# Kernel optimization log

Measured on AMD Instinct MI355X. Metric: run time of the kernel, lower is better.

The kernel has to match this reference:

```python
import jax, jax.numpy as jnp
import numpy as np

N, F_IN, H, C, E = 100000, 128, 128, 40, 600000


def setup_inputs() -> dict:
    key = jax.random.key(0)
    ks = jax.random.split(key, 20)
    s = 0.05
    inp = {
        "x": jax.random.normal(ks[0], (N, F_IN), jnp.float32),
        "edge_index": jax.random.randint(ks[1], (2, E), 0, N, jnp.int64),
        "importance": jnp.ones((F_IN,), jnp.float32),
        "W1": jax.random.normal(ks[2], (H, F_IN), jnp.float32) * s,
        "bl1": jax.random.normal(ks[3], (H,), jnp.float32) * s,
        "bc1": jnp.zeros((H,), jnp.float32),
        "W2": jax.random.normal(ks[4], (H, H), jnp.float32) * s,
        "bl2": jax.random.normal(ks[5], (H,), jnp.float32) * s,
        "bc2": jnp.zeros((H,), jnp.float32),
        "W3": jax.random.normal(ks[6], (H, H), jnp.float32) * s,
        "bl3": jax.random.normal(ks[7], (H,), jnp.float32) * s,
        "bc3": jnp.zeros((H,), jnp.float32),
        "Wlin1": jax.random.normal(ks[8], (H, H), jnp.float32) * s,
        "blin1": jax.random.normal(ks[9], (H,), jnp.float32) * s,
        "Wlin2": jax.random.normal(ks[10], (C, H), jnp.float32) * s,
        "blin2": jax.random.normal(ks[11], (C,), jnp.float32) * s,
    }
    return inp


def balanced_conv(x, W, bl, bc, row, col):
    # lin, then symmetric-normalized message, mean-aggregated over targets
    n = x.shape[0]
    h = x @ W.T + bl                                   # [N, H]
    loops = jnp.arange(n)
    r = jnp.concatenate([row, loops])                  # sources (x_j index)
    c = jnp.concatenate([col, loops])                  # targets
    deg = jnp.zeros((n,), x.dtype).at[c].add(1.0)      # degree(col) incl. self-loops
    dinv = deg ** -0.5
    norm = dinv[r] * dinv[c]                           # [E+N]
    msg = norm[:, None] * h[r]                         # gather + scale
    agg = jnp.zeros((n, h.shape[1]), x.dtype).at[c].add(msg)  # scatter-add
    return agg / deg[:, None] + bc                     # mean aggr + bias


def reference(x, edge_index, importance, W1, bl1, bc1, W2, bl2, bc2,
              W3, bl3, bc3, Wlin1, blin1, Wlin2, blin2):
    row, col = edge_index[0], edge_index[1]
    h = x * importance
    h = jax.nn.relu(balanced_conv(h, W1, bl1, bc1, row, col))
    h = jax.nn.relu(balanced_conv(h, W2, bl2, bc2, row, col))
    h = jax.nn.relu(balanced_conv(h, W3, bl3, bc3, row, col))
    h = jax.nn.relu(h @ Wlin1.T + blin1)
    h = h @ Wlin2.T + blin2
    return jax.nn.log_softmax(h, axis=-1)
```

## Files before the change

kernel.cpp:

```cpp
#include <hip/hip_runtime.h>
#include <hip/hip_bf16.h>

#define F 128
#define C_CLS 40
#define NWSPLIT 35
#define ELLCAP 32

typedef __attribute__((ext_vector_type(8))) short short8;
typedef __attribute__((ext_vector_type(4))) float float4v;
typedef unsigned short ushort;

__device__ inline float bf2f(ushort u) {
  unsigned int x = ((unsigned int)u) << 16;
  return __builtin_bit_cast(float, x);
}
__device__ inline ushort f2bf(float f) {
  __hip_bfloat16 h = __float2bfloat16(f);
  return __builtin_bit_cast(ushort, h);
}
__device__ inline void split_bf16(float f, ushort& hi, ushort& lo) {
  hi = f2bf(f);
  lo = f2bf(f - bf2f(hi));
}
__device__ inline int swz(int lane) { return lane ^ ((lane >> 4) & 3); }

__global__ __launch_bounds__(256) void setup_kernel(
    const float* __restrict__ W1, const float* __restrict__ imp,
    const float* __restrict__ W2, const float* __restrict__ W3,
    const float* __restrict__ Wl1, const float* __restrict__ Wh2,
    ushort* __restrict__ WhP,
    ushort* __restrict__ W2hH, ushort* __restrict__ W2lH,
    const int* __restrict__ row, const int* __restrict__ col,
    int* __restrict__ cnt, int* __restrict__ ell,
    int ne, int n) {
  int b = blockIdx.x;
  if (b < NWSPLIT) {
    int ci = b * 256 + threadIdx.x;
    if (ci < 8192) {
      const float* src[4] = {W1, W2, W3, Wl1};
      int p = ci >> 11, c = ci & 2047;
      int kc = c >> 10, ct = (c >> 7) & 7, ks = (c >> 6) & 1, ln = c & 63;
      int dl = swz(ln);
      int colw = ct * 16 + (dl & 15);
      int k = kc * 64 + ks * 32 + (dl >> 4) * 8;
      float4 f0 = *(const float4*)&src[p][(size_t)colw * F + k];
      float4 f1 = *(const float4*)&src[p][(size_t)colw * F + k + 4];
      float v[8] = {f0.x, f0.y, f0.z, f0.w, f1.x, f1.y, f1.z, f1.w};
      if (p == 0) {
        float4 i0 = *(const float4*)&imp[k];
        float4 i1 = *(const float4*)&imp[k + 4];
        v[0] *= i0.x; v[1] *= i0.y; v[2] *= i0.z; v[3] *= i0.w;
        v[4] *= i1.x; v[5] *= i1.y; v[6] *= i1.z; v[7] *= i1.w;
      }
      ushort hi[8];
#pragma unroll
      for (int j = 0; j < 8; ++j) hi[j] = f2bf(v[j]);
      *(short8*)&WhP[(size_t)ci * 8] = *(short8*)hi;
    } else if (ci < 8192 + 768) {
      int c = ci - 8192;
      int ct = c >> 8, ks = (c >> 6) & 3, ln = c & 63;
      int colw = ct * 16 + (ln & 15);
      int k = ks * 32 + (ln >> 4) * 8;
      float v[8];
      if (colw < C_CLS) {
        float4 f0 = *(const float4*)&Wh2[(size_t)colw * F + k];
        float4 f1 = *(const float4*)&Wh2[(size_t)colw * F + k + 4];
        v[0] = f0.x; v[1] = f0.y; v[2] = f0.z; v[3] = f0.w;
        v[4] = f1.x; v[5] = f1.y; v[6] = f1.z; v[7] = f1.w;
      } else {
#pragma unroll
        for (int j = 0; j < 8; ++j) v[j] = 0.f;
      }
      ushort hi[8], lo[8];
#pragma unroll
      for (int j = 0; j < 8; ++j) split_bf16(v[j], hi[j], lo[j]);
      *(short8*)&W2hH[(size_t)c * 8] = *(short8*)hi;
      *(short8*)&W2lH[(size_t)c * 8] = *(short8*)lo;
    }
  } else {
    int e = (b - NWSPLIT) * 256 + threadIdx.x;
    if (e < ne) {
      int r = row[e], c = col[e];
      int p = atomicAdd(&cnt[c], 1);
      if (p < ELLCAP) ell[(size_t)c * ELLCAP + p] = r;
    }
  }
}

template <bool F32IN>
__global__ __launch_bounds__(256, 2) void gemm_any(const void* __restrict__ INv,
    const ushort* __restrict__ Wh,
    const float* __restrict__ bias, ushort* __restrict__ OUT, int nrows, int relu,
    int nbMain, const int* __restrict__ cntv, float* __restrict__ dinvv,
    float* __restrict__ invdegv, int n) {
  __shared__ ushort sWh[16384];
  if (blockIdx.x >= nbMain) {
    int i = (blockIdx.x - nbMain) * 256 + threadIdx.x;
    if (i < n) {
      float d = (float)(cntv[i] + 1);
      dinvv[i] = rsqrtf(d);
      invdegv[i] = 1.0f / d;
    }
    return;
  }
  const int t = threadIdx.x;
  const int rbase = blockIdx.x * 256;
  const int w = t >> 6, lane = t & 63;
  const int quad = lane >> 4, cl = lane & 15;

#pragma unroll
  for (int pp = 0; pp < 8; ++pp) {
    int ci = t + pp * 256;
    *(short8*)&sWh[ci * 8] = *(const short8*)&Wh[(size_t)ci * 8];
  }
  __syncthreads();

  float4v acc[4][8];
#pragma unroll
  for (int nt = 0; nt < 4; ++nt)
#pragma unroll
    for (int mt = 0; mt < 8; ++mt) acc[nt][mt] = (float4v){0.f, 0.f, 0.f, 0.f};

  const int sl = swz(lane);
  const int nrow0 = rbase + w * 64 + cl;
#pragma unroll
  for (int ks = 0; ks < 4; ++ks) {
    short8 b[4];
#pragma unroll
    for (int nt = 0; nt < 4; ++nt) {
      int gr = nrow0 + nt * 16;
      if (gr < nrows) {
        if (F32IN) {
          const float* INf = (const float*)INv;
          float4 f0 = *(const float4*)&INf[(size_t)gr * F + ks * 32 + quad * 8];
          float4 f1 = *(const float4*)&INf[(size_t)gr * F + ks * 32 + quad * 8 + 4];
          ushort h[8] = {f2bf(f0.x), f2bf(f0.y), f2bf(f0.z), f2bf(f0.w),
                         f2bf(f1.x), f2bf(f1.y), f2bf(f1.z), f2bf(f1.w)};
          b[nt] = *(short8*)h;
        } else {
          const ushort* IN = (const ushort*)INv;
          b[nt] = *(const short8*)&IN[(size_t)gr * F + ks * 32 + quad * 8];
        }
      } else {
        b[nt] = (short8){0, 0, 0, 0, 0, 0, 0, 0};
      }
    }
    const int base = ((ks >> 1) * 1024 + (ks & 1) * 64 + sl) * 8;
#pragma unroll
    for (int mt = 0; mt < 8; ++mt) {
      short8 a_h = *(short8*)&sWh[base + mt * 128 * 8];
#pragma unroll
      for (int nt = 0; nt < 4; ++nt)
        acc[nt][mt] = __builtin_amdgcn_mfma_f32_16x16x32_bf16(a_h, b[nt], acc[nt][mt], 0, 0, 0);
    }
  }
#pragma unroll
  for (int mt = 0; mt < 8; ++mt) {
    float4 bv = *(const float4*)&bias[mt * 16 + quad * 4];
#pragma unroll
    for (int nt = 0; nt < 4; ++nt) {
      int gr = nrow0 + nt * 16;
      if (gr < nrows) {
        float v0 = acc[nt][mt][0] + bv.x;
        float v1 = acc[nt][mt][1] + bv.y;
        float v2 = acc[nt][mt][2] + bv.z;
        float v3 = acc[nt][mt][3] + bv.w;
        if (relu) {
          v0 = fmaxf(v0, 0.f); v1 = fmaxf(v1, 0.f);
          v2 = fmaxf(v2, 0.f); v3 = fmaxf(v3, 0.f);
        }
        ushort o[4] = {f2bf(v0), f2bf(v1), f2bf(v2), f2bf(v3)};
        *(ushort4*)&OUT[(size_t)gr * F + mt * 16 + quad * 4] = *(ushort4*)o;
      }
    }
  }
}

__global__ __launch_bounds__(256) void gather_kernel(const int* __restrict__ cntv,
    const int* __restrict__ ell, const ushort* __restrict__ B,
    const float* __restrict__ dinv, const float* __restrict__ invdeg,
    const float* __restrict__ bc, ushort* __restrict__ A, int n) {
  int node = blockIdx.x * 16 + (threadIdx.x >> 4);
  if (node >= n) return;
  int j = (threadIdx.x & 15) * 8;
  int cnt = cntv[node];
  int lim = cnt < ELLCAP ? cnt : ELLCAP;
  float dc = dinv[node];
  const int4* ep = (const int4*)&ell[(size_t)node * ELLCAP];
  float a0[8] = {0, 0, 0, 0, 0, 0, 0, 0};
  float a1[8] = {0, 0, 0, 0, 0, 0, 0, 0};
  float a2[8] = {0, 0, 0, 0, 0, 0, 0, 0};
  float a3[8] = {0, 0, 0, 0, 0, 0, 0, 0};
  for (int base = 0; base < lim; base += 4) {
    int4 rr = ep[base >> 2];
    bool p1 = base + 1 < lim, p2 = base + 2 < lim, p3 = base + 3 < lim;
    int r1 = p1 ? rr.y : rr.x;
    int r2 = p2 ? rr.z : rr.x;
    int r3 = p3 ? rr.w : rr.x;
    float g0 = dinv[rr.x];
    float g1 = p1 ? dinv[r1] : 0.f;
    float g2 = p2 ? dinv[r2] : 0.f;
    float g3 = p3 ? dinv[r3] : 0.f;
    short8 v0 = *(const short8*)&B[(size_t)rr.x * F + j];
    short8 v1 = *(const short8*)&B[(size_t)r1 * F + j];
    short8 v2 = *(const short8*)&B[(size_t)r2 * F + j];
    short8 v3 = *(const short8*)&B[(size_t)r3 * F + j];
#pragma unroll
    for (int q = 0; q < 8; ++q) {
      a0[q] += g0 * bf2f((ushort)v0[q]);
      a1[q] += g1 * bf2f((ushort)v1[q]);
      a2[q] += g2 * bf2f((ushort)v2[q]);
      a3[q] += g3 * bf2f((ushort)v3[q]);
    }
  }
  float id = invdeg[node];
  short8 sv = *(const short8*)&B[(size_t)node * F + j];
  float4 b0 = *(const float4*)&bc[j];
  float4 b1 = *(const float4*)&bc[j + 4];
  float bcv[8] = {b0.x, b0.y, b0.z, b0.w, b1.x, b1.y, b1.z, b1.w};
  ushort o[8];
#pragma unroll
  for (int q = 0; q < 8; ++q) {
    float s = dc * ((a0[q] + a1[q]) + (a2[q] + a3[q]));
    o[q] = f2bf(fmaxf((s + bf2f((ushort)sv[q]) * id) * id + bcv[q], 0.f));
  }
  *(short8*)&A[(size_t)node * F + j] = *(short8*)o;
}

__global__ __launch_bounds__(256, 2) void head_fused(const ushort* __restrict__ X,
    const ushort* __restrict__ Wl1h, const float* __restrict__ bl,
    const ushort* __restrict__ W2h, const ushort* __restrict__ W2l,
    const float* __restrict__ b2, float* __restrict__ out, int nrows) {
  __shared__ ushort sWh[16384];
  __shared__ ushort sW2h[6144], sW2l[6144];
  __shared__ ushort sH[8192];
  __shared__ float b2s[48];
  const int t = threadIdx.x;
#pragma unroll
  for (int pp = 0; pp < 8; ++pp) {
    int ci = t + pp * 256;
    *(short8*)&sWh[ci * 8] = *(const short8*)&Wl1h[(size_t)ci * 8];
  }
#pragma unroll
  for (int pp = 0; pp < 3; ++pp) {
    int c = t + pp * 256;
    *(short8*)&sW2h[c * 8] = *(const short8*)&W2h[(size_t)c * 8];
    *(short8*)&sW2l[c * 8] = *(const short8*)&W2l[(size_t)c * 8];
  }
  if (t < 48) b2s[t] = (t < C_CLS) ? b2[t] : -1e30f;
  __syncthreads();

  const int w = t >> 6, lane = t & 63;
  const int quad = lane >> 4, cl = lane & 15;
  const int sl = swz(lane);
  const int row0 = (blockIdx.x * 4 + w) * 16;
  char* sHb = (char*)sH;

  float4v acc1[8];
#pragma unroll
  for (int mt = 0; mt < 8; ++mt) acc1[mt] = (float4v){0.f, 0.f, 0.f, 0.f};
  const int gr1 = row0 + cl;
#pragma unroll
  for (int ks = 0; ks < 4; ++ks) {
    short8 b;
    if (gr1 < nrows) b = *(const short8*)&X[(size_t)gr1 * F + ks * 32 + quad * 8];
    else b = (short8){0, 0, 0, 0, 0, 0, 0, 0};
    const int base = ((ks >> 1) * 1024 + (ks & 1) * 64 + sl) * 8;
#pragma unroll
    for (int mt = 0; mt < 8; ++mt) {
      short8 a_h = *(short8*)&sWh[base + mt * 128 * 8];
      acc1[mt] = __builtin_amdgcn_mfma_f32_16x16x32_bf16(a_h, b, acc1[mt], 0, 0, 0);
    }
  }
#pragma unroll
  for (int mt = 0; mt < 8; ++mt) {
    float4 bv = *(const float4*)&bl[mt * 16 + quad * 4];
    ushort o[4];
    o[0] = f2bf(fmaxf(acc1[mt][0] + bv.x, 0.f));
    o[1] = f2bf(fmaxf(acc1[mt][1] + bv.y, 0.f));
    o[2] = f2bf(fmaxf(acc1[mt][2] + bv.z, 0.f));
    o[3] = f2bf(fmaxf(acc1[mt][3] + bv.w, 0.f));
    int ch = (mt * 2 + (quad >> 1)) ^ cl;
    *(ushort4*)&sHb[w * 4096 + cl * 256 + ch * 16 + (quad & 1) * 8] = *(ushort4*)o;
  }
  __syncthreads();

  float4v acc[3];
#pragma unroll
  for (int ct = 0; ct < 3; ++ct) acc[ct] = (float4v){0.f, 0.f, 0.f, 0.f};
#pragma unroll
  for (int ks = 0; ks < 4; ++ks) {
    int ch2 = (ks * 4 + quad) ^ cl;
    short8 a = *(short8*)&sHb[w * 4096 + cl * 256 + ch2 * 16];
#pragma unroll
    for (int ct = 0; ct < 3; ++ct) {
      int chunk = ((ct * 4 + ks) * 64 + lane) * 8;
      short8 b_h = *(short8*)&sW2h[chunk];
      short8 b_l = *(short8*)&sW2l[chunk];
      acc[ct] = __builtin_amdgcn_mfma_f32_16x16x32_bf16(a, b_h, acc[ct], 0, 0, 0);
      acc[ct] = __builtin_amdgcn_mfma_f32_16x16x32_bf16(a, b_l, acc[ct], 0, 0, 0);
    }
  }

  float b0 = b2s[cl], b1 = b2s[16 + cl], b2v = b2s[32 + cl];
  float lse[4];
#pragma unroll
  for (int reg = 0; reg < 4; ++reg) {
    float v0 = acc[0][reg] + b0;
    float v1 = acc[1][reg] + b1;
    float v2 = acc[2][reg] + b2v;
    acc[0][reg] = v0; acc[1][reg] = v1; acc[2][reg] = v2;
    float m = fmaxf(fmaxf(v0, v1), v2);
#pragma unroll
    for (int o = 1; o < 16; o <<= 1) m = fmaxf(m, __shfl_xor(m, o));
    float s = __expf(v0 - m) + __expf(v1 - m) + __expf(v2 - m);
#pragma unroll
    for (int o = 1; o < 16; o <<= 1) s += __shfl_xor(s, o);
    lse[reg] = logf(s) + m;
  }
#pragma unroll
  for (int reg = 0; reg < 4; ++reg) {
    int gr = row0 + quad * 4 + reg;
    if (gr < nrows) {
      out[(size_t)gr * C_CLS + cl] = acc[0][reg] - lse[reg];
      out[(size_t)gr * C_CLS + 16 + cl] = acc[1][reg] - lse[reg];
      if (cl < 8) out[(size_t)gr * C_CLS + 32 + cl] = acc[2][reg] - lse[reg];
    }
  }
}

extern "C" void kernel_launch(void* const* d_in, const int* in_sizes, int n_in,
                              void* d_out, int out_size, void* d_ws, size_t ws_size,
                              hipStream_t stream) {
  const float* x    = (const float*)d_in[0];
  const int*   ei   = (const int*)d_in[1];
  const float* imp  = (const float*)d_in[2];
  const float* W1   = (const float*)d_in[3];
  const float* bl1  = (const float*)d_in[4];
  const float* bc1  = (const float*)d_in[5];
  const float* W2   = (const float*)d_in[6];
  const float* bl2  = (const float*)d_in[7];
  const float* bc2  = (const float*)d_in[8];
  const float* W3   = (const float*)d_in[9];
  const float* bl3  = (const float*)d_in[10];
  const float* bc3  = (const float*)d_in[11];
  const float* Wl1  = (const float*)d_in[12];
  const float* bli1 = (const float*)d_in[13];
  const float* Wl2  = (const float*)d_in[14];
  const float* bli2 = (const float*)d_in[15];
  float* out = (float*)d_out;

  const int N = in_sizes[0] / F;
  const int E = in_sizes[1] / 2;

  ushort* A16 = (ushort*)d_ws;
  ushort* B16 = A16 + (size_t)N * F;
  ushort* WhP = B16 + (size_t)N * F;
  ushort* W2hH = WhP + 65536;
  ushort* W2lH = W2hH + 6144;
  float* dinv = (float*)(W2lH + 6144);
  float* invdeg = dinv + N;
  int*   cnt  = (int*)(invdeg + N);
  int*   ell  = cnt + N;

  const int* rowv = ei;
  const int* colv = ei + E;

  int nbN  = (N + 255) / 256;
  int nbE  = (E + 255) / 256;
  int nbG  = (N + 255) / 256;
  int nbGa = (N + 15) / 16;
  int nbHd = (N + 63) / 64;

  hipMemsetAsync(cnt, 0, (size_t)N * sizeof(int), stream);
  setup_kernel<<<NWSPLIT + nbE, 256, 0, stream>>>(
      W1, imp, W2, W3, Wl1, Wl2, WhP, W2hH, W2lH, rowv, colv, cnt, ell, E, N);

  gemm_any<true><<<nbG + nbN, 256, 0, stream>>>(x, WhP, bl1, B16, N, 0,
                                                nbG, cnt, dinv, invdeg, N);
  gather_kernel<<<nbGa, 256, 0, stream>>>(cnt, ell, B16, dinv, invdeg, bc1, A16, N);

  gemm_any<false><<<nbG, 256, 0, stream>>>(A16, WhP + 16384, bl2, B16, N, 0,
                                           nbG, nullptr, nullptr, nullptr, 0);
  gather_kernel<<<nbGa, 256, 0, stream>>>(cnt, ell, B16, dinv, invdeg, bc2, A16, N);

  gemm_any<false><<<nbG, 256, 0, stream>>>(A16, WhP + 32768, bl3, B16, N, 0,
                                           nbG, nullptr, nullptr, nullptr, 0);
  gather_kernel<<<nbGa, 256, 0, stream>>>(cnt, ell, B16, dinv, invdeg, bc3, A16, N);

  head_fused<<<nbHd, 256, 0, stream>>>(A16, WhP + 49152, bli1, W2hH, W2lH, bli2, out, N);
}
```

Baseline: 321.3 us.

## Fuse neighbor aggregation with the layer GEMM by aggregating before transforming

Each conv layer is reordered so neighbor features are aggregated first, then multiplied by W in the same kernel. The linear bias is folded in through the sum of normalization weights, so the separate GEMM pass and its intermediate write and read are removed. Degree normalization is recomputed from the edge counts on the fly instead of being stored, and the fp32-to-bf16 conversion of x moves into the setup kernel. The cost is more per-thread gather work: each thread now handles 32 features per node instead of 8, with lower per-node parallelism during the gather phase.

```diff
diff --git a/kernel.cpp b/kernel.cpp
--- a/kernel.cpp
+++ b/kernel.cpp
@@ -28,11 +28,12 @@
     const float* __restrict__ W1, const float* __restrict__ imp,
     const float* __restrict__ W2, const float* __restrict__ W3,
     const float* __restrict__ Wl1, const float* __restrict__ Wh2,
+    const float* __restrict__ x,
     ushort* __restrict__ WhP,
     ushort* __restrict__ W2hH, ushort* __restrict__ W2lH,
     const int* __restrict__ row, const int* __restrict__ col,
-    int* __restrict__ cnt, int* __restrict__ ell,
-    int ne, int n) {
+    int* __restrict__ cnt, int* __restrict__ ell, ushort* __restrict__ X16,
+    int ne, int n, int nbE) {
   int b = blockIdx.x;
   if (b < NWSPLIT) {
     int ci = b * 256 + threadIdx.x;
@@ -77,154 +78,134 @@
       *(short8*)&W2hH[(size_t)c * 8] = *(short8*)hi;
       *(short8*)&W2lH[(size_t)c * 8] = *(short8*)lo;
     }
-  } else {
+  } else if (b < NWSPLIT + nbE) {
     int e = (b - NWSPLIT) * 256 + threadIdx.x;
     if (e < ne) {
       int r = row[e], c = col[e];
       int p = atomicAdd(&cnt[c], 1);
       if (p < ELLCAP) ell[(size_t)c * ELLCAP + p] = r;
     }
-  }
-}
-
-template <bool F32IN>
-__global__ __launch_bounds__(256, 2) void gemm_any(const void* __restrict__ INv,
-    const ushort* __restrict__ Wh,
-    const float* __restrict__ bias, ushort* __restrict__ OUT, int nrows, int relu,
-    int nbMain, const int* __restrict__ cntv, float* __restrict__ dinvv,
-    float* __restrict__ invdegv, int n) {
+  } else {
+    int i = (b - NWSPLIT - nbE) * 2048 + threadIdx.x * 8;
+    if (i < n * F) {
+      float4 f0 = *(const float4*)&x[i];
+      float4 f1 = *(const float4*)&x[i + 4];
+      ushort o[8] = {f2bf(f0.x), f2bf(f0.y), f2bf(f0.z), f2bf(f0.w),
+                     f2bf(f1.x), f2bf(f1.y), f2bf(f1.z), f2bf(f1.w)};
+      *(short8*)&X16[i] = *(short8*)o;
+    }
+  }
+}
+
+__global__ __launch_bounds__(256, 2) void conv_fused(
+    const int* __restrict__ cnt, const int* __restrict__ ell,
+    const ushort* __restrict__ Xin, const ushort* __restrict__ Wh,
+    const float* __restrict__ bl, const float* __restrict__ bc,
+    ushort* __restrict__ OUT, int n) {
   __shared__ ushort sWh[16384];
-  if (blockIdx.x >= nbMain) {
-    int i = (blockIdx.x - nbMain) * 256 + threadIdx.x;
-    if (i < n) {
-      float d = (float)(cntv[i] + 1);
-      dinvv[i] = rsqrtf(d);
-      invdegv[i] = 1.0f / d;
-    }
-    return;
-  }
   const int t = threadIdx.x;
-  const int rbase = blockIdx.x * 256;
-  const int w = t >> 6, lane = t & 63;
-  const int quad = lane >> 4, cl = lane & 15;
-
 #pragma unroll
   for (int pp = 0; pp < 8; ++pp) {
     int ci = t + pp * 256;
     *(short8*)&sWh[ci * 8] = *(const short8*)&Wh[(size_t)ci * 8];
   }
-  __syncthreads();
-
-  float4v acc[4][8];
-#pragma unroll
-  for (int nt = 0; nt < 4; ++nt)
-#pragma unroll
-    for (int mt = 0; mt < 8; ++mt) acc[nt][mt] = (float4v){0.f, 0.f, 0.f, 0.f};
-
-  const int sl = swz(lane);
-  const int nrow0 = rbase + w * 64 + cl;
-#pragma unroll
-  for (int ks = 0; ks < 4; ++ks) {
-    short8 b[4];
-#pragma unroll
-    for (int nt = 0; nt < 4; ++nt) {
-      int gr = nrow0 + nt * 16;
-      if (gr < nrows) {
-        if (F32IN) {
-          const float* INf = (const float*)INv;
-          float4 f0 = *(const float4*)&INf[(size_t)gr * F + ks * 32 + quad * 8];
-          float4 f1 = *(const float4*)&INf[(size_t)gr * F + ks * 32 + quad * 8 + 4];
-          ushort h[8] = {f2bf(f0.x), f2bf(f0.y), f2bf(f0.z), f2bf(f0.w),
-                         f2bf(f1.x), f2bf(f1.y), f2bf(f1.z), f2bf(f1.w)};
-          b[nt] = *(short8*)h;
-        } else {
-          const ushort* IN = (const ushort*)INv;
-          b[nt] = *(const short8*)&IN[(size_t)gr * F + ks * 32 + quad * 8];
-        }
-      } else {
-        b[nt] = (short8){0, 0, 0, 0, 0, 0, 0, 0};
-      }
-    }
-    const int base = ((ks >> 1) * 1024 + (ks & 1) * 64 + sl) * 8;
-#pragma unroll
-    for (int mt = 0; mt < 8; ++mt) {
-      short8 a_h = *(short8*)&sWh[base + mt * 128 * 8];
-#pragma unroll
-      for (int nt = 0; nt < 4; ++nt)
-        acc[nt][mt] = __builtin_amdgcn_mfma_f32_16x16x32_bf16(a_h, b[nt], acc[nt][mt], 0, 0, 0);
-    }
-  }
-#pragma unroll
-  for (int mt = 0; mt < 8; ++mt) {
-    float4 bv = *(const float4*)&bias[mt * 16 + quad * 4];
-#pragma unroll
-    for (int nt = 0; nt < 4; ++nt) {
-      int gr = nrow0 + nt * 16;
-      if (gr < nrows) {
-        float v0 = acc[nt][mt][0] + bv.x;
-        float v1 = acc[nt][mt][1] + bv.y;
-        float v2 = acc[nt][mt][2] + bv.z;
-        float v3 = acc[nt][mt][3] + bv.w;
-        if (relu) {
-          v0 = fmaxf(v0, 0.f); v1 = fmaxf(v1, 0.f);
-          v2 = fmaxf(v2, 0.f); v3 = fmaxf(v3, 0.f);
-        }
-        ushort o[4] = {f2bf(v0), f2bf(v1), f2bf(v2), f2bf(v3)};
-        *(ushort4*)&OUT[(size_t)gr * F + mt * 16 + quad * 4] = *(ushort4*)o;
-      }
-    }
-  }
-}
-
-__global__ __launch_bounds__(256) void gather_kernel(const int* __restrict__ cntv,
-    const int* __restrict__ ell, const ushort* __restrict__ B,
-    const float* __restrict__ dinv, const float* __restrict__ invdeg,
-    const float* __restrict__ bc, ushort* __restrict__ A, int n) {
-  int node = blockIdx.x * 16 + (threadIdx.x >> 4);
-  if (node >= n) return;
-  int j = (threadIdx.x & 15) * 8;
-  int cnt = cntv[node];
-  int lim = cnt < ELLCAP ? cnt : ELLCAP;
-  float dc = dinv[node];
+  const int w = t >> 6, lane = t & 63, quad = lane >> 4, cl = lane & 15;
+  const int node = blockIdx.x * 64 + w * 16 + cl;
+
+  float acc[4][8];
+#pragma unroll
+  for (int ks = 0; ks < 4; ++ks)
+#pragma unroll
+    for (int q = 0; q < 8; ++q) acc[ks][q] = 0.f;
+
+  float gsum = 0.f, dc = 0.f, id = 0.f;
+  int lim = 0;
+  if (node < n) {
+    int cv = cnt[node];
+    float d = (float)(cv + 1);
+    dc = rsqrtf(d);
+    id = 1.0f / d;
+    lim = cv < ELLCAP ? cv : ELLCAP;
+  }
   const int4* ep = (const int4*)&ell[(size_t)node * ELLCAP];
-  float a0[8] = {0, 0, 0, 0, 0, 0, 0, 0};
-  float a1[8] = {0, 0, 0, 0, 0, 0, 0, 0};
-  float a2[8] = {0, 0, 0, 0, 0, 0, 0, 0};
-  float a3[8] = {0, 0, 0, 0, 0, 0, 0, 0};
+  const int qoff = quad * 8;
+
   for (int base = 0; base < lim; base += 4) {
     int4 rr = ep[base >> 2];
     bool p1 = base + 1 < lim, p2 = base + 2 < lim, p3 = base + 3 < lim;
     int r1 = p1 ? rr.y : rr.x;
     int r2 = p2 ? rr.z : rr.x;
     int r3 = p3 ? rr.w : rr.x;
-    float g0 = dinv[rr.x];
-    float g1 = p1 ? dinv[r1] : 0.f;
-    float g2 = p2 ? dinv[r2] : 0.f;
-    float g3 = p3 ? dinv[r3] : 0.f;
-    short8 v0 = *(const short8*)&B[(size_t)rr.x * F + j];
-    short8 v1 = *(const short8*)&B[(size_t)r1 * F + j];
-    short8 v2 = *(const short8*)&B[(size_t)r2 * F + j];
-    short8 v3 = *(const short8*)&B[(size_t)r3 * F + j];
-#pragma unroll
-    for (int q = 0; q < 8; ++q) {
-      a0[q] += g0 * bf2f((ushort)v0[q]);
-      a1[q] += g1 * bf2f((ushort)v1[q]);
-      a2[q] += g2 * bf2f((ushort)v2[q]);
-      a3[q] += g3 * bf2f((ushort)v3[q]);
-    }
-  }
-  float id = invdeg[node];
-  short8 sv = *(const short8*)&B[(size_t)node * F + j];
-  float4 b0 = *(const float4*)&bc[j];
-  float4 b1 = *(const float4*)&bc[j + 4];
-  float bcv[8] = {b0.x, b0.y, b0.z, b0.w, b1.x, b1.y, b1.z, b1.w};
-  ushort o[8];
-#pragma unroll
-  for (int q = 0; q < 8; ++q) {
-    float s = dc * ((a0[q] + a1[q]) + (a2[q] + a3[q]));
-    o[q] = f2bf(fmaxf((s + bf2f((ushort)sv[q]) * id) * id + bcv[q], 0.f));
-  }
-  *(short8*)&A[(size_t)node * F + j] = *(short8*)o;
+    float g0 = rsqrtf((float)(cnt[rr.x] + 1));
+    float g1 = p1 ? rsqrtf((float)(cnt[r1] + 1)) : 0.f;
+    float g2 = p2 ? rsqrtf((float)(cnt[r2] + 1)) : 0.f;
+    float g3 = p3 ? rsqrtf((float)(cnt[r3] + 1)) : 0.f;
+    gsum += (g0 + g1) + (g2 + g3);
+    const ushort* q0 = &Xin[(size_t)rr.x * F + qoff];
+    const ushort* q1 = &Xin[(size_t)r1 * F + qoff];
+    const ushort* q2 = &Xin[(size_t)r2 * F + qoff];
+    const ushort* q3 = &Xin[(size_t)r3 * F + qoff];
+#pragma unroll
+    for (int ks = 0; ks < 4; ++ks) {
+      short8 v0 = *(const short8*)&q0[ks * 32];
+      short8 v1 = *(const short8*)&q1[ks * 32];
+      short8 v2 = *(const short8*)&q2[ks * 32];
+      short8 v3 = *(const short8*)&q3[ks * 32];
+#pragma unroll
+      for (int q = 0; q < 8; ++q) {
+        float t0 = g0 * bf2f((ushort)v0[q]) + g1 * bf2f((ushort)v1[q]);
+        float t1 = g2 * bf2f((ushort)v2[q]) + g3 * bf2f((ushort)v3[q]);
+        acc[ks][q] += t0 + t1;
+      }
+    }
+  }
+
+  short8 sfrag[4];
+  float wsum = dc * gsum + id;
+  if (node < n) {
+    const ushort* sq = &Xin[(size_t)node * F + qoff];
+#pragma unroll
+    for (int ks = 0; ks < 4; ++ks) {
+      short8 sv = *(const short8*)&sq[ks * 32];
+      ushort o[8];
+#pragma unroll
+      for (int q = 0; q < 8; ++q)
+        o[q] = f2bf(dc * acc[ks][q] + id * bf2f((ushort)sv[q]));
+      sfrag[ks] = *(short8*)o;
+    }
+  } else {
+#pragma unroll
+    for (int ks = 0; ks < 4; ++ks) sfrag[ks] = (short8){0, 0, 0, 0, 0, 0, 0, 0};
+  }
+  __syncthreads();
+
+  float4v co[8];
+#pragma unroll
+  for (int mt = 0; mt < 8; ++mt) co[mt] = (float4v){0.f, 0.f, 0.f, 0.f};
+  const int sl = swz(lane);
+#pragma unroll
+  for (int ks = 0; ks < 4; ++ks) {
+    const int base2 = ((ks >> 1) * 1024 + (ks & 1) * 64 + sl) * 8;
+#pragma unroll
+    for (int mt = 0; mt < 8; ++mt) {
+      short8 a_h = *(short8*)&sWh[base2 + mt * 128 * 8];
+      co[mt] = __builtin_amdgcn_mfma_f32_16x16x32_bf16(a_h, sfrag[ks], co[mt], 0, 0, 0);
+    }
+  }
+
+  if (node < n) {
+#pragma unroll
+    for (int mt = 0; mt < 8; ++mt) {
+      float4 blv = *(const float4*)&bl[mt * 16 + quad * 4];
+      float4 bcv = *(const float4*)&bc[mt * 16 + quad * 4];
+      ushort o[4];
+      o[0] = f2bf(fmaxf((co[mt][0] + wsum * blv.x) * id + bcv.x, 0.f));
+      o[1] = f2bf(fmaxf((co[mt][1] + wsum * blv.y) * id + bcv.y, 0.f));
+      o[2] = f2bf(fmaxf((co[mt][2] + wsum * blv.z) * id + bcv.z, 0.f));
+      o[3] = f2bf(fmaxf((co[mt][3] + wsum * blv.w) * id + bcv.w, 0.f));
+      *(ushort4*)&OUT[(size_t)node * F + mt * 16 + quad * 4] = *(ushort4*)o;
+    }
+  }
 }
 
 __global__ __launch_bounds__(256, 2) void head_fused(const ushort* __restrict__ X,
@@ -358,35 +339,25 @@
   ushort* WhP = B16 + (size_t)N * F;
   ushort* W2hH = WhP + 65536;
   ushort* W2lH = W2hH + 6144;
-  float* dinv = (float*)(W2lH + 6144);
-  float* invdeg = dinv + N;
-  int*   cnt  = (int*)(invdeg + N);
+  int*   cnt  = (int*)(W2lH + 6144);
   int*   ell  = cnt + N;
 
   const int* rowv = ei;
   const int* colv = ei + E;
 
-  int nbN  = (N + 255) / 256;
   int nbE  = (E + 255) / 256;
-  int nbG  = (N + 255) / 256;
-  int nbGa = (N + 15) / 16;
+  int nbX  = (N * F + 2047) / 2048;
+  int nbCv = (N + 63) / 64;
   int nbHd = (N + 63) / 64;
 
   hipMemsetAsync(cnt, 0, (size_t)N * sizeof(int), stream);
-  setup_kernel<<<NWSPLIT + nbE, 256, 0, stream>>>(
-      W1, imp, W2, W3, Wl1, Wl2, WhP, W2hH, W2lH, rowv, colv, cnt, ell, E, N);
-
-  gemm_any<true><<<nbG + nbN, 256, 0, stream>>>(x, WhP, bl1, B16, N, 0,
-                                                nbG, cnt, dinv, invdeg, N);
-  gather_kernel<<<nbGa, 256, 0, stream>>>(cnt, ell, B16, dinv, invdeg, bc1, A16, N);
-
-  gemm_any<false><<<nbG, 256, 0, stream>>>(A16, WhP + 16384, bl2, B16, N, 0,
-                                           nbG, nullptr, nullptr, nullptr, 0);
-  gather_kernel<<<nbGa, 256, 0, stream>>>(cnt, ell, B16, dinv, invdeg, bc2, A16, N);
-
-  gemm_any<false><<<nbG, 256, 0, stream>>>(A16, WhP + 32768, bl3, B16, N, 0,
-                                           nbG, nullptr, nullptr, nullptr, 0);
-  gather_kernel<<<nbGa, 256, 0, stream>>>(cnt, ell, B16, dinv, invdeg, bc3, A16, N);
+  setup_kernel<<<NWSPLIT + nbE + nbX, 256, 0, stream>>>(
+      W1, imp, W2, W3, Wl1, Wl2, x, WhP, W2hH, W2lH, rowv, colv, cnt, ell, B16,
+      E, N, nbE);
+
+  conv_fused<<<nbCv, 256, 0, stream>>>(cnt, ell, B16, WhP,         bl1, bc1, A16, N);
+  conv_fused<<<nbCv, 256, 0, stream>>>(cnt, ell, A16, WhP + 16384, bl2, bc2, B16, N);
+  conv_fused<<<nbCv, 256, 0, stream>>>(cnt, ell, B16, WhP + 32768, bl3, bc3, A16, N);
 
   head_fused<<<nbHd, 256, 0, stream>>>(A16, WhP + 49152, bli1, W2hH, W2lH, bli2, out, N);
 }
```

Measured after the change: 329.3 us. 2.5% more time.
